# Kernel optimization log

Hardware: AMD Instinct MI355X
Metric: run time of the kernel (lower is better)

Reference implementation:

```python
import jax, jax.numpy as jnp
import numpy as np

NEG_SLOPE = 0.1

def lrelu(x):
    return jnp.where(x >= 0, x, NEG_SLOPE * x)

def conv1d(x, w, b, stride=2):
    # x: [N, C_in, W], w: [C_out, C_in, K], VALID padding, given stride
    y = jax.lax.conv_general_dilated(x, w, (stride,), 'VALID',
                                     dimension_numbers=('NCH', 'OIH', 'NCH'))
    return y + b[None, :, None]

def setup_inputs() -> dict:
    key = jax.random.key(0)
    ks = jax.random.split(key, 16)
    N_NODES = 50000
    N_EDGES = 4950000
    POS_C, CONV_C, CONV_W = 3, 3, 151
    HID, OUT = 256, 1
    W2 = 37  # width after two stride-2 k=3 convs on 151
    IN_G = POS_C + W2  # 40

    def lin_init(k, fan_out, fan_in):
        s = 1.0 / np.sqrt(fan_in)
        k1, k2 = jax.random.split(k)
        return (jax.random.uniform(k1, (fan_out, fan_in), jnp.float32, -s, s),
                jax.random.uniform(k2, (fan_out,), jnp.float32, -s, s))

    pose = jax.random.normal(ks[0], (N_NODES, POS_C), jnp.float32)
    views = jax.random.normal(ks[1], (N_NODES, CONV_C, CONV_W), jnp.float32)
    edge_index = jax.random.randint(ks[2], (2, N_EDGES), 0, N_NODES, jnp.int64)

    # encoder1: Conv1d(3 -> 9, k=3, s=2); encoder2: Conv1d(9 -> 1, k=3, s=2)
    s1 = 1.0 / np.sqrt(CONV_C * 3)
    w_e1 = jax.random.uniform(ks[3], (CONV_C ** 2, CONV_C, 3), jnp.float32, -s1, s1)
    b_e1 = jax.random.uniform(ks[4], (CONV_C ** 2,), jnp.float32, -s1, s1)
    s2 = 1.0 / np.sqrt(CONV_C ** 2 * 3)
    w_e2 = jax.random.uniform(ks[5], (1, CONV_C ** 2, 3), jnp.float32, -s2, s2)
    b_e2 = jax.random.uniform(ks[6], (1,), jnp.float32, -s2, s2)

    # GraphConv: lin_rel (with bias) on aggregated neighbors, lin_root (no bias) on self
    w_rel, b_rel = lin_init(ks[7], HID, IN_G)
    w_root, _ = lin_init(ks[8], HID, IN_G)

    w_l1, b_l1 = lin_init(ks[9], HID, HID)
    w_l2, b_l2 = lin_init(ks[10], HID, HID)
    w_l3, b_l3 = lin_init(ks[11], HID, HID)
    w_pred, b_pred = lin_init(ks[12], OUT, HID)

    return dict(pose=pose, views=views, edge_index=edge_index,
                w_e1=w_e1, b_e1=b_e1, w_e2=w_e2, b_e2=b_e2,
                w_rel=w_rel, b_rel=b_rel, w_root=w_root,
                w_l1=w_l1, b_l1=b_l1, w_l2=w_l2, b_l2=b_l2,
                w_l3=w_l3, b_l3=b_l3, w_pred=w_pred, b_pred=b_pred)

def reference(pose, views, edge_index, w_e1, b_e1, w_e2, b_e2,
              w_rel, b_rel, w_root,
              w_l1, b_l1, w_l2, b_l2, w_l3, b_l3, w_pred, b_pred):
    n_nodes = pose.shape[0]
    # view encoder
    v = lrelu(conv1d(views, w_e1, b_e1))          # [N, 9, 75]
    v = lrelu(conv1d(v, w_e2, b_e2))              # [N, 1, 37]
    x = jnp.concatenate([pose, v[:, 0, :]], axis=1)  # [N, 40]
    # GraphConv (aggr='add'): out = lin_rel(sum_{j->i} x_j) + lin_root(x_i)
    src, dst = edge_index[0], edge_index[1]
    agg = jax.ops.segment_sum(x[src], dst, num_segments=n_nodes)  # [N, 40]
    h = lrelu(agg @ w_rel.T + b_rel + x @ w_root.T)               # [N, 256]
    # MLP stack (dropout is identity in eval mode)
    h = lrelu(h @ w_l1.T + b_l1)
    h = lrelu(h @ w_l2.T + b_l2)
    h = lrelu(h @ w_l3.T + b_l3)
    return h @ w_pred.T + b_pred  # [N, 1]
```

## Files before the change

### kernel.cpp

```cpp
#include <hip/hip_runtime.h>
#include <hip/hip_fp16.h>

#define NEG_SLOPE 0.1f
__device__ __forceinline__ float lrelu(float v) { return fmaxf(v, NEG_SLOPE * v); }

constexpr int CAP = 8704;
constexpr int EPB = 8192;

typedef __attribute__((ext_vector_type(8))) short short8;
typedef __attribute__((ext_vector_type(4))) float f32x4;

__device__ __forceinline__ unsigned short f2bf(float f) {
    union { float f; unsigned u; } v; v.f = f;
    const unsigned r = v.u + 0x7FFF + ((v.u >> 16) & 1);
    return (unsigned short)(r >> 16);
}
__device__ __forceinline__ float bf2f(unsigned short h) {
    union { unsigned u; float f; } v; v.u = ((unsigned)h) << 16;
    return v.f;
}

__global__ __launch_bounds__(256) void encoder_kernel(
        const float* __restrict__ pose,
        const float* __restrict__ views,
        const float* __restrict__ w1, const float* __restrict__ b1,
        const float* __restrict__ w2, const float* __restrict__ b2,
        const float* __restrict__ w_l1, const float* __restrict__ w_l2,
        const float* __restrict__ w_l3, const float* __restrict__ w_rel,
        const float* __restrict__ w_root,
        unsigned short* __restrict__ Wb1, unsigned short* __restrict__ Wb2,
        unsigned short* __restrict__ Wb3, unsigned short* __restrict__ Wg,
        int* __restrict__ gcur,
        unsigned short* __restrict__ xHi, unsigned short* __restrict__ xLo,
        __half* __restrict__ xh, int N)
{
    __shared__ float s_w1[81];
    __shared__ float s_b1[9];
    __shared__ float s_w2[27];
    __shared__ float s_b2[1];
    __shared__ float s_c1[4][9][80];

    const int t = threadIdx.x;

    if (blockIdx.x < 256) {
        const int i = blockIdx.x * 256 + t;
        Wb1[i] = f2bf(w_l1[i]);
        Wb2[i] = f2bf(w_l2[i]);
        Wb3[i] = f2bf(w_l3[i]);
        if (i < 40960) {
            const int m = i / 160, c = i % 160;
            const int k = c % 80;
            const float v = (k < 40) ? w_rel[m * 40 + k] : w_root[m * 40 + (k - 40)];
            Wg[i] = f2bf(v);
        }
        if (i < 1024) gcur[i] = 0;
        if (i < 40) xh[(size_t)N * 40 + i] = __float2half(0.f);
    }

    if (t < 81) s_w1[t] = w1[t];
    if (t >= 96 && t < 105) s_b1[t - 96] = b1[t - 96];
    if (t >= 128 && t < 155) s_w2[t - 128] = w2[t - 128];
    if (t == 240) s_b2[0] = b2[0];
    __syncthreads();

    const int nb = blockIdx.x * 4;

    #pragma unroll
    for (int pass = 0; pass < 2; pass++) {
        const int task = pass * 256 + t;
        if (task < 300) {
            const int ln = task / 75;
            const int p  = task % 75;
            const int n  = min(nb + ln, N - 1);
            const float* __restrict__ vin = views + (size_t)n * 453 + 2 * p;
            float e[3], o[3], e1[3];
            #pragma unroll
            for (int ic = 0; ic < 3; ic++) {
                const float* ci = vin + ic * 151;
                e[ic] = ci[0]; o[ic] = ci[1]; e1[ic] = ci[2];
            }
            const int didx = (p & 1) * 40 + (p >> 1);
            #pragma unroll
            for (int oc = 0; oc < 9; oc++) {
                float v = s_b1[oc];
                #pragma unroll
                for (int ic = 0; ic < 3; ic++)
                    v += s_w1[oc * 9 + ic * 3 + 0] * e[ic]
                       + s_w1[oc * 9 + ic * 3 + 1] * o[ic]
                       + s_w1[oc * 9 + ic * 3 + 2] * e1[ic];
                s_c1[ln][oc][didx] = lrelu(v);
            }
        }
    }
    __syncthreads();

    if (t < 160) {
        const int ln = t / 40, f = t % 40;
        const int n  = min(nb + ln, N - 1);
        float outv;
        if (f < 3) {
            outv = pose[(size_t)n * 3 + f];
        } else {
            const int ow = f - 3;
            float v = s_b2[0];
            #pragma unroll
            for (int ic = 0; ic < 9; ic++)
                v += s_w2[ic * 3 + 0] * s_c1[ln][ic][ow]
                   + s_w2[ic * 3 + 1] * s_c1[ln][ic][40 + ow]
                   + s_w2[ic * 3 + 2] * s_c1[ln][ic][ow + 1];
            outv = lrelu(v);
        }
        const unsigned short hi = f2bf(outv);
        const unsigned short lo = f2bf(outv - bf2f(hi));
        xHi[(size_t)n * 40 + f] = hi;
        xLo[(size_t)n * 40 + f] = lo;
        xh[(size_t)n * 40 + f] = __float2half(outv);
    }
}

__global__ __launch_bounds__(512) void bin_kernel(
        const int* __restrict__ ei, int* __restrict__ gcur,
        int* __restrict__ pairs, int E, int NB)
{
    __shared__ int s_hist[1024];
    __shared__ int s_loff[1024];
    __shared__ int s_base[1024];
    __shared__ int s_wave8[8];
    __shared__ int s_pk[EPB];
    __shared__ unsigned short s_bkt[EPB];
    const int t = threadIdx.x;
    const int lane = t & 63, wid = t >> 6;
    const int e0 = blockIdx.x * EPB + t * 16;
    const int tot = min(E - blockIdx.x * EPB, EPB);

    for (int i = t; i < 1024; i += 512) s_hist[i] = 0;
    __syncthreads();

    int pk[16], mt[16];
    auto proc = [&](int j, int sv, int dv) {
        const int b = dv >> 6;
        const int r = atomicAdd(&s_hist[b], 1);
        pk[j] = sv * 80 | ((dv & 63) << 22);
        mt[j] = b | (r << 10);
    };

    if (e0 + 16 <= E) {
        #pragma unroll
        for (int q = 0; q < 4; q++) {
            const int4 sv = *(const int4*)(ei + e0 + 4 * q);
            const int4 dv = *(const int4*)(ei + E + e0 + 4 * q);
            proc(4 * q + 0, sv.x, dv.x);
            proc(4 * q + 1, sv.y, dv.y);
            proc(4 * q + 2, sv.z, dv.z);
            proc(4 * q + 3, sv.w, dv.w);
        }
    } else {
        #pragma unroll
        for (int j = 0; j < 16; j++) {
            mt[j] = -1;
            const int e = e0 + j;
            if (e < E) proc(j, ei[e], ei[E + e]);
        }
    }
    __syncthreads();

    int carry = 0;
    #pragma unroll
    for (int base = 0; base < 1024; base += 512) {
        const int i = base + t;
        const int v = s_hist[i];
        int sc = v;
        #pragma unroll
        for (int d = 1; d < 64; d <<= 1) {
            const int u = __shfl_up(sc, d);
            if (lane >= d) sc += u;
        }
        if (lane == 63) s_wave8[wid] = sc;
        __syncthreads();
        if (wid == 0) {
            int wv = (lane < 8) ? s_wave8[lane] : 0;
            #pragma unroll
            for (int d = 1; d < 8; d <<= 1) {
                const int u = __shfl_up(wv, d);
                if (lane >= d) wv += u;
            }
            if (lane < 8) s_wave8[lane] = wv;
        }
        __syncthreads();
        const int waveoff = (wid > 0) ? s_wave8[wid - 1] : 0;
        s_loff[i] = carry + waveoff + sc - v;
        const int chunk_tot = s_wave8[7];
        __syncthreads();
        carry += chunk_tot;
    }

    for (int i = t; i < NB; i += 512) {
        const int c = s_hist[i];
        if (c > 0) s_base[i] = atomicAdd(&gcur[i], c);
    }
    __syncthreads();

    #pragma unroll
    for (int j = 0; j < 16; j++) {
        if (mt[j] >= 0) {
            const int b = mt[j] & 1023;
            const int pos = s_loff[b] + (mt[j] >> 10);
            s_pk[pos] = pk[j];
            s_bkt[pos] = (unsigned short)b;
        }
    }
    __syncthreads();

    for (int i = t; i < tot; i += 512) {
        const int b = s_bkt[i];
        const int p = s_base[b] + (i - s_loff[b]);
        if (p < CAP) pairs[b * CAP + p] = s_pk[i];
    }
}

__global__ void bucket_sort_kernel(const int* __restrict__ gcur,
                                   const int* __restrict__ pairs,
                                   int* __restrict__ sorted,
                                   int* __restrict__ node_start,
                                   int* __restrict__ node_cnt, int N)
{
    __shared__ int s_cnt[64], s_off[64], s_cur[64];
    const int b = blockIdx.x;
    const int t = threadIdx.x;
    const int cnt = min(gcur[b], CAP);
    const int* __restrict__ pr = pairs + b * CAP;
    int* __restrict__ so = sorted + (size_t)b * CAP;

    if (t < 64) s_cnt[t] = 0;
    __syncthreads();
    for (int i = t; i < cnt; i += 256)
        atomicAdd(&s_cnt[pr[i] >> 22], 1);
    __syncthreads();

    if (t < 64) {
        const int c = s_cnt[t];
        const int p = ((c + 23) / 24) * 24;
        int sc = p;
        #pragma unroll
        for (int d = 1; d < 64; d <<= 1) {
            const int u = __shfl_up(sc, d);
            if (t >= d) sc += u;
        }
        const int excl = sc - p;
        s_off[t] = excl;
        s_cur[t] = excl;
        node_start[b * 64 + t] = b * CAP + excl;
        node_cnt[b * 64 + t] = c;
    }
    __syncthreads();

    if (t < 64) {
        const int e0 = s_off[t] + s_cnt[t];
        const int e1 = s_off[t] + ((s_cnt[t] + 23) / 24) * 24;
        for (int i = e0; i < e1 && i < CAP; i++) so[i] = N * 80;
    }
    for (int i = t; i < cnt; i += 256) {
        const int p = pr[i];
        const int pos = atomicAdd(&s_cur[p >> 22], 1);
        if (pos < CAP) so[pos] = p & 0x3FFFFF;
    }
}

__global__ void gather_sum_kernel(const int* __restrict__ sorted,
                                  const int* __restrict__ node_start,
                                  const int* __restrict__ node_cnt,
                                  const __half* __restrict__ xh,
                                  unsigned short* __restrict__ aggHi,
                                  unsigned short* __restrict__ aggLo, int N)
{
    const int n = blockIdx.x * 4 + (threadIdx.x >> 6);
    const int lane = threadIdx.x & 63;
    if (n >= N) return;

    const int start = node_start[n];
    const int cntp = ((node_cnt[n] + 23) / 24) * 24;
    const int slot = min(lane / 10, 5);
    const int f4 = lane % 10;
    const int* __restrict__ srt = sorted + start + slot;
    const char* __restrict__ xb = (const char*)xh + f4 * 8;

    float ax = 0.f, ay = 0.f, az = 0.f, aw = 0.f;
    for (int e = 0; e < cntp; e += 24) {
        const int o0 = srt[e];
        const int o1 = srt[e + 6];
        const int o2 = srt[e + 12];
        const int o3 = srt[e + 18];
        const uint2 u0 = *(const uint2*)(xb + o0);
        const uint2 u1 = *(const uint2*)(xb + o1);
        const uint2 u2 = *(const uint2*)(xb + o2);
        const uint2 u3 = *(const uint2*)(xb + o3);
        union { unsigned u; __half2 h; } c;
        float2 f;
        c.u = u0.x; f = __half22float2(c.h); ax += f.x; ay += f.y;
        c.u = u0.y; f = __half22float2(c.h); az += f.x; aw += f.y;
        c.u = u1.x; f = __half22float2(c.h); ax += f.x; ay += f.y;
        c.u = u1.y; f = __half22float2(c.h); az += f.x; aw += f.y;
        c.u = u2.x; f = __half22float2(c.h); ax += f.x; ay += f.y;
        c.u = u2.y; f = __half22float2(c.h); az += f.x; aw += f.y;
        c.u = u3.x; f = __half22float2(c.h); ax += f.x; ay += f.y;
        c.u = u3.y; f = __half22float2(c.h); az += f.x; aw += f.y;
    }

    float rx = ax, ry = ay, rz = az, rw = aw;
    #pragma unroll
    for (int s = 10; s <= 50; s += 10) {
        rx += __shfl(ax, f4 + s);
        ry += __shfl(ay, f4 + s);
        rz += __shfl(az, f4 + s);
        rw += __shfl(aw, f4 + s);
    }
    if (lane < 10) {
        ushort4 hi, lo;
        hi.x = f2bf(rx); lo.x = f2bf(rx - bf2f(hi.x));
        hi.y = f2bf(ry); lo.y = f2bf(ry - bf2f(hi.y));
        hi.z = f2bf(rz); lo.z = f2bf(rz - bf2f(hi.z));
        hi.w = f2bf(rw); lo.w = f2bf(rw - bf2f(hi.w));
        *(ushort4*)(aggHi + (size_t)n * 40 + f4 * 4) = hi;
        *(ushort4*)(aggLo + (size_t)n * 40 + f4 * 4) = lo;
    }
}

__global__ void graphconv_mfma_kernel(const unsigned short* __restrict__ aggHi,
                                      const unsigned short* __restrict__ aggLo,
                                      const unsigned short* __restrict__ xHi,
                                      const unsigned short* __restrict__ xLo,
                                      const unsigned short* __restrict__ Wg,
                                      const float* __restrict__ b,
                                      unsigned short* __restrict__ C, int N)
{
    __shared__ __align__(16) unsigned short aT[64 * 168];
    const int t = threadIdx.x;
    const int n0 = blockIdx.x * 64;
    const int wave = t >> 6, lane = t & 63, q = lane >> 4, l16 = lane & 15;

    for (int u = t; u < 640; u += 256) {
        const int row = u / 10, c = (u % 10) * 4;
        const int srow = min(n0 + row, N - 1);
        const size_t off = (size_t)srow * 40 + c;
        const ushort4 ha = *(const ushort4*)(aggHi + off);
        const ushort4 hx = *(const ushort4*)(xHi + off);
        const ushort4 la = *(const ushort4*)(aggLo + off);
        const ushort4 lx = *(const ushort4*)(xLo + off);
        unsigned short* rp = aT + row * 168;
        *(ushort4*)(rp + c)       = ha;
        *(ushort4*)(rp + 40 + c)  = hx;
        *(ushort4*)(rp + 80 + c)  = la;
        *(ushort4*)(rp + 120 + c) = lx;
    }
    __syncthreads();

    f32x4 acc[4][4] = {};
    for (int k0 = 0; k0 < 160; k0 += 32) {
        short8 af[4], wf[4];
        #pragma unroll
        for (int nt = 0; nt < 4; nt++)
            af[nt] = *(const short8*)(aT + (nt * 16 + l16) * 168 + k0 + q * 8);
        #pragma unroll
        for (int mt = 0; mt < 4; mt++)
            wf[mt] = *(const short8*)(Wg + (wave * 64 + mt * 16 + l16) * 160 + k0 + q * 8);
        #pragma unroll
        for (int nt = 0; nt < 4; nt++)
            #pragma unroll
            for (int mt = 0; mt < 4; mt++)
                acc[nt][mt] = __builtin_amdgcn_mfma_f32_16x16x32_bf16(af[nt], wf[mt], acc[nt][mt], 0, 0, 0);
    }

    float bias[4];
    #pragma unroll
    for (int mt = 0; mt < 4; mt++) bias[mt] = b[wave * 64 + mt * 16 + l16];

    #pragma unroll
    for (int nt = 0; nt < 4; nt++)
        #pragma unroll
        for (int r = 0; r < 4; r++) {
            const int row = n0 + nt * 16 + q * 4 + r;
            if (row >= N) continue;
            #pragma unroll
            for (int mt = 0; mt < 4; mt++) {
                const int col = wave * 64 + mt * 16 + l16;
                C[(size_t)row * 256 + col] = f2bf(lrelu(acc[nt][mt][r] + bias[mt]));
            }
        }
}

__global__ void mlp_mfma_kernel(const unsigned short* __restrict__ A,
                                const unsigned short* __restrict__ W,
                                const float* __restrict__ b,
                                unsigned short* __restrict__ C, int N)
{
    __shared__ __align__(16) unsigned short aT[64 * 264];
    const int t = threadIdx.x;
    const int n0 = blockIdx.x * 64;
    const int wave = t >> 6, lane = t & 63, q = lane >> 4, l16 = lane & 15;

    #pragma unroll
    for (int i = 0; i < 8; i++) {
        const int u = t + 256 * i;
        const int row = u >> 5, c16 = u & 31;
        const int srow = min(n0 + row, N - 1);
        *(uint4*)(aT + row * 264 + c16 * 8) = *(const uint4*)(A + (size_t)srow * 256 + c16 * 8);
    }
    __syncthreads();

    f32x4 acc[4][4] = {};
    const unsigned short* wbase = W + (wave * 64 + l16) * 256 + q * 8;
    for (int k0 = 0; k0 < 256; k0 += 32) {
        short8 af[4], wf[4];
        #pragma unroll
        for (int nt = 0; nt < 4; nt++)
            af[nt] = *(const short8*)(aT + (nt * 16 + l16) * 264 + k0 + q * 8);
        #pragma unroll
        for (int mt = 0; mt < 4; mt++)
            wf[mt] = *(const short8*)(wbase + mt * 16 * 256 + k0);
        #pragma unroll
        for (int nt = 0; nt < 4; nt++)
            #pragma unroll
            for (int mt = 0; mt < 4; mt++)
                acc[nt][mt] = __builtin_amdgcn_mfma_f32_16x16x32_bf16(af[nt], wf[mt], acc[nt][mt], 0, 0, 0);
    }

    float bias[4];
    #pragma unroll
    for (int mt = 0; mt < 4; mt++) bias[mt] = b[wave * 64 + mt * 16 + l16];

    #pragma unroll
    for (int nt = 0; nt < 4; nt++)
        #pragma unroll
        for (int r = 0; r < 4; r++) {
            const int row = n0 + nt * 16 + q * 4 + r;
            if (row >= N) continue;
            #pragma unroll
            for (int mt = 0; mt < 4; mt++) {
                const int col = wave * 64 + mt * 16 + l16;
                C[(size_t)row * 256 + col] = f2bf(lrelu(acc[nt][mt][r] + bias[mt]));
            }
        }
}

__global__ void mlp_pred_kernel(const unsigned short* __restrict__ A,
                                const unsigned short* __restrict__ W,
                                const float* __restrict__ b,
                                const float* __restrict__ w_pred,
                                const float* __restrict__ b_pred,
                                float* __restrict__ out, int N)
{
    __shared__ __align__(16) unsigned short aT[64 * 264];
    __shared__ float s_part[4][64];
    const int t = threadIdx.x;
    const int n0 = blockIdx.x * 64;
    const int wave = t >> 6, lane = t & 63, q = lane >> 4, l16 = lane & 15;

    #pragma unroll
    for (int i = 0; i < 8; i++) {
        const int u = t + 256 * i;
        const int row = u >> 5, c16 = u & 31;
        const int srow = min(n0 + row, N - 1);
        *(uint4*)(aT + row * 264 + c16 * 8) = *(const uint4*)(A + (size_t)srow * 256 + c16 * 8);
    }
    __syncthreads();

    f32x4 acc[4][4] = {};
    const unsigned short* wbase = W + (wave * 64 + l16) * 256 + q * 8;
    for (int k0 = 0; k0 < 256; k0 += 32) {
        short8 af[4], wf[4];
        #pragma unroll
        for (int nt = 0; nt < 4; nt++)
            af[nt] = *(const short8*)(aT + (nt * 16 + l16) * 264 + k0 + q * 8);
        #pragma unroll
        for (int mt = 0; mt < 4; mt++)
            wf[mt] = *(const short8*)(wbase + mt * 16 * 256 + k0);
        #pragma unroll
        for (int nt = 0; nt < 4; nt++)
            #pragma unroll
            for (int mt = 0; mt < 4; mt++)
                acc[nt][mt] = __builtin_amdgcn_mfma_f32_16x16x32_bf16(af[nt], wf[mt], acc[nt][mt], 0, 0, 0);
    }

    float bias[4], wp[4];
    #pragma unroll
    for (int mt = 0; mt < 4; mt++) {
        const int col = wave * 64 + mt * 16 + l16;
        bias[mt] = b[col];
        wp[mt] = w_pred[col];
    }

    #pragma unroll
    for (int nt = 0; nt < 4; nt++)
        #pragma unroll
        for (int r = 0; r < 4; r++) {
            float p = 0.f;
            #pragma unroll
            for (int mt = 0; mt < 4; mt++)
                p += lrelu(acc[nt][mt][r] + bias[mt]) * wp[mt];
            p += __shfl_xor(p, 1);
            p += __shfl_xor(p, 2);
            p += __shfl_xor(p, 4);
            p += __shfl_xor(p, 8);
            if (l16 == 0) s_part[wave][nt * 16 + q * 4 + r] = p;
        }
    __syncthreads();

    if (t < 64) {
        const int row = n0 + t;
        if (row < N)
            out[row] = s_part[0][t] + s_part[1][t] + s_part[2][t] + s_part[3][t] + b_pred[0];
    }
}

extern "C" void kernel_launch(void* const* d_in, const int* in_sizes, int n_in,
                              void* d_out, int out_size, void* d_ws, size_t ws_size,
                              hipStream_t stream)
{
    const float* pose   = (const float*)d_in[0];
    const float* views  = (const float*)d_in[1];
    const int*   ei     = (const int*)d_in[2];
    const float* w_e1   = (const float*)d_in[3];
    const float* b_e1   = (const float*)d_in[4];
    const float* w_e2   = (const float*)d_in[5];
    const float* b_e2   = (const float*)d_in[6];
    const float* w_rel  = (const float*)d_in[7];
    const float* b_rel  = (const float*)d_in[8];
    const float* w_root = (const float*)d_in[9];
    const float* w_l1   = (const float*)d_in[10];
    const float* b_l1   = (const float*)d_in[11];
    const float* w_l2   = (const float*)d_in[12];
    const float* b_l2   = (const float*)d_in[13];
    const float* w_l3   = (const float*)d_in[14];
    const float* b_l3   = (const float*)d_in[15];
    const float* w_pred = (const float*)d_in[16];
    const float* b_pred = (const float*)d_in[17];
    float* out = (float*)d_out;

    const int N = in_sizes[0] / 3;
    const int E = in_sizes[2] / 2;
    const int NB = (N + 63) >> 6;
    const int NBLK = (N + 63) / 64;

    unsigned short* xHi = (unsigned short*)d_ws;
    unsigned short* xLo = xHi + (size_t)N * 40;
    unsigned short* aggHi = xLo + (size_t)N * 40;
    unsigned short* aggLo = aggHi + (size_t)N * 40;
    __half* xh = (__half*)(aggLo + (size_t)N * 40);
    int* pairs  = (int*)(xh + (size_t)(N + 1) * 40 + 24);
    int* sorted = pairs + (size_t)NB * CAP;
    unsigned short* hb0 = (unsigned short*)pairs;
    unsigned short* hb1 = (unsigned short*)sorted;
    int* gcur       = sorted + (size_t)NB * CAP;
    int* node_start = gcur + 1024;
    int* node_cnt   = node_start + NB * 64;
    unsigned short* Wb1 = (unsigned short*)(node_cnt + NB * 64);
    unsigned short* Wb2 = Wb1 + 256 * 256;
    unsigned short* Wb3 = Wb2 + 256 * 256;
    unsigned short* Wg  = Wb3 + 256 * 256;

    encoder_kernel<<<(N + 3) / 4, 256, 0, stream>>>(
        pose, views, w_e1, b_e1, w_e2, b_e2,
        w_l1, w_l2, w_l3, w_rel, w_root,
        Wb1, Wb2, Wb3, Wg, gcur, xHi, xLo, xh, N);

    bin_kernel<<<(E + EPB - 1) / EPB, 512, 0, stream>>>(ei, gcur, pairs, E, NB);
    bucket_sort_kernel<<<NB, 256, 0, stream>>>(gcur, pairs, sorted, node_start, node_cnt, N);
    gather_sum_kernel<<<NB * 16, 256, 0, stream>>>(sorted, node_start, node_cnt, xh, aggHi, aggLo, N);

    graphconv_mfma_kernel<<<NBLK, 256, 0, stream>>>(aggHi, aggLo, xHi, xLo, Wg, b_rel, hb0, N);
    mlp_mfma_kernel<<<NBLK, 256, 0, stream>>>(hb0, Wb1, b_l1, hb1, N);
    mlp_mfma_kernel<<<NBLK, 256, 0, stream>>>(hb1, Wb2, b_l2, hb0, N);
    mlp_pred_kernel<<<NBLK, 256, 0, stream>>>(hb0, Wb3, b_l3, w_pred, b_pred, out, N);
}
```

Before: 391.2 us.

## Fuse graphconv and MLP GEMMs into one kernel, merge encoder with edge binning

Chains the graphconv GEMM and the three MLP layers inside one kernel, keeping each 64-row activation tile in LDS between layers. This removes the global write and read of the 256-wide hidden activations and three kernel launches. It also merges the encoder and edge-binning kernels into one launch using block-index dispatch over a shared LDS union, and zeroes the bucket counters with a memset. The trade-off is that the GEMM chain is serialized per block with extra barriers, and the merged launch uses larger blocks and more LDS for encoder blocks.

```diff
diff --git a/kernel.cpp b/kernel.cpp
--- a/kernel.cpp
+++ b/kernel.cpp
@@ -20,9 +20,21 @@
     return v.f;
 }
 
-__global__ __launch_bounds__(256) void encoder_kernel(
-        const float* __restrict__ pose,
-        const float* __restrict__ views,
+struct BinSmem {
+    int hist[1024], loff[1024], base[1024];
+    int wave8[8];
+    int pk[EPB];
+    unsigned short bkt[EPB];
+};
+struct EncSmem {
+    float w1[81], b1v[9], w2[27], b2v[1];
+    float c1[8][9][80];
+};
+
+__global__ __launch_bounds__(512) void enc_bin_kernel(
+        const int* __restrict__ ei, int* __restrict__ gcur,
+        int* __restrict__ pairs, int E, int NB, int NBIN,
+        const float* __restrict__ pose, const float* __restrict__ views,
         const float* __restrict__ w1, const float* __restrict__ b1,
         const float* __restrict__ w2, const float* __restrict__ b2,
         const float* __restrict__ w_l1, const float* __restrict__ w_l2,
@@ -30,20 +42,109 @@
         const float* __restrict__ w_root,
         unsigned short* __restrict__ Wb1, unsigned short* __restrict__ Wb2,
         unsigned short* __restrict__ Wb3, unsigned short* __restrict__ Wg,
-        int* __restrict__ gcur,
         unsigned short* __restrict__ xHi, unsigned short* __restrict__ xLo,
         __half* __restrict__ xh, int N)
 {
-    __shared__ float s_w1[81];
-    __shared__ float s_b1[9];
-    __shared__ float s_w2[27];
-    __shared__ float s_b2[1];
-    __shared__ float s_c1[4][9][80];
-
+    __shared__ __align__(16) char smem_raw[sizeof(BinSmem)];
     const int t = threadIdx.x;
 
-    if (blockIdx.x < 256) {
-        const int i = blockIdx.x * 256 + t;
+    if (blockIdx.x < (unsigned)NBIN) {
+        BinSmem& sm = *reinterpret_cast<BinSmem*>(smem_raw);
+        const int lane = t & 63, wid = t >> 6;
+        const int e0 = blockIdx.x * EPB + t * 16;
+        const int tot = min(E - (int)blockIdx.x * EPB, EPB);
+
+        for (int i = t; i < 1024; i += 512) sm.hist[i] = 0;
+        __syncthreads();
+
+        int pk[16], mt[16];
+        auto proc = [&](int j, int sv, int dv) {
+            const int b = dv >> 6;
+            const int r = atomicAdd(&sm.hist[b], 1);
+            pk[j] = sv * 80 | ((dv & 63) << 22);
+            mt[j] = b | (r << 10);
+        };
+
+        if (e0 + 16 <= E) {
+            #pragma unroll
+            for (int q = 0; q < 4; q++) {
+                const int4 sv = *(const int4*)(ei + e0 + 4 * q);
+                const int4 dv = *(const int4*)(ei + E + e0 + 4 * q);
+                proc(4 * q + 0, sv.x, dv.x);
+                proc(4 * q + 1, sv.y, dv.y);
+                proc(4 * q + 2, sv.z, dv.z);
+                proc(4 * q + 3, sv.w, dv.w);
+            }
+        } else {
+            #pragma unroll
+            for (int j = 0; j < 16; j++) {
+                mt[j] = -1;
+                const int e = e0 + j;
+                if (e < E) proc(j, ei[e], ei[E + e]);
+            }
+        }
+        __syncthreads();
+
+        int carry = 0;
+        #pragma unroll
+        for (int base = 0; base < 1024; base += 512) {
+            const int i = base + t;
+            const int v = sm.hist[i];
+            int sc = v;
+            #pragma unroll
+            for (int d = 1; d < 64; d <<= 1) {
+                const int u = __shfl_up(sc, d);
+                if (lane >= d) sc += u;
+            }
+            if (lane == 63) sm.wave8[wid] = sc;
+            __syncthreads();
+            if (wid == 0) {
+                int wv = (lane < 8) ? sm.wave8[lane] : 0;
+                #pragma unroll
+                for (int d = 1; d < 8; d <<= 1) {
+                    const int u = __shfl_up(wv, d);
+                    if (lane >= d) wv += u;
+                }
+                if (lane < 8) sm.wave8[lane] = wv;
+            }
+            __syncthreads();
+            const int waveoff = (wid > 0) ? sm.wave8[wid - 1] : 0;
+            sm.loff[i] = carry + waveoff + sc - v;
+            const int chunk_tot = sm.wave8[7];
+            __syncthreads();
+            carry += chunk_tot;
+        }
+
+        for (int i = t; i < NB; i += 512) {
+            const int c = sm.hist[i];
+            if (c > 0) sm.base[i] = atomicAdd(&gcur[i], c);
+        }
+        __syncthreads();
+
+        #pragma unroll
+        for (int j = 0; j < 16; j++) {
+            if (mt[j] >= 0) {
+                const int b = mt[j] & 1023;
+                const int pos = sm.loff[b] + (mt[j] >> 10);
+                sm.pk[pos] = pk[j];
+                sm.bkt[pos] = (unsigned short)b;
+            }
+        }
+        __syncthreads();
+
+        for (int i = t; i < tot; i += 512) {
+            const int b = sm.bkt[i];
+            const int p = sm.base[b] + (i - sm.loff[b]);
+            if (p < CAP) pairs[b * CAP + p] = sm.pk[i];
+        }
+        return;
+    }
+
+    EncSmem& sm = *reinterpret_cast<EncSmem*>(smem_raw);
+    const int eb = blockIdx.x - NBIN;
+
+    if (eb < 128) {
+        const int i = eb * 512 + t;
         Wb1[i] = f2bf(w_l1[i]);
         Wb2[i] = f2bf(w_l2[i]);
         Wb3[i] = f2bf(w_l3[i]);
@@ -53,22 +154,21 @@
             const float v = (k < 40) ? w_rel[m * 40 + k] : w_root[m * 40 + (k - 40)];
             Wg[i] = f2bf(v);
         }
-        if (i < 1024) gcur[i] = 0;
-        if (i < 40) xh[(size_t)N * 40 + i] = __float2half(0.f);
-    }
-
-    if (t < 81) s_w1[t] = w1[t];
-    if (t >= 96 && t < 105) s_b1[t - 96] = b1[t - 96];
-    if (t >= 128 && t < 155) s_w2[t - 128] = w2[t - 128];
-    if (t == 240) s_b2[0] = b2[0];
+        if (eb == 0 && t < 40) xh[(size_t)N * 40 + t] = __float2half(0.f);
+    }
+
+    if (t < 81) sm.w1[t] = w1[t];
+    if (t >= 96 && t < 105) sm.b1v[t - 96] = b1[t - 96];
+    if (t >= 128 && t < 155) sm.w2[t - 128] = w2[t - 128];
+    if (t == 240) sm.b2v[0] = b2[0];
     __syncthreads();
 
-    const int nb = blockIdx.x * 4;
+    const int nb = eb * 8;
 
     #pragma unroll
     for (int pass = 0; pass < 2; pass++) {
-        const int task = pass * 256 + t;
-        if (task < 300) {
+        const int task = pass * 512 + t;
+        if (task < 600) {
             const int ln = task / 75;
             const int p  = task % 75;
             const int n  = min(nb + ln, N - 1);
@@ -82,19 +182,19 @@
             const int didx = (p & 1) * 40 + (p >> 1);
             #pragma unroll
             for (int oc = 0; oc < 9; oc++) {
-                float v = s_b1[oc];
+                float v = sm.b1v[oc];
                 #pragma unroll
                 for (int ic = 0; ic < 3; ic++)
-                    v += s_w1[oc * 9 + ic * 3 + 0] * e[ic]
-                       + s_w1[oc * 9 + ic * 3 + 1] * o[ic]
-                       + s_w1[oc * 9 + ic * 3 + 2] * e1[ic];
-                s_c1[ln][oc][didx] = lrelu(v);
+                    v += sm.w1[oc * 9 + ic * 3 + 0] * e[ic]
+                       + sm.w1[oc * 9 + ic * 3 + 1] * o[ic]
+                       + sm.w1[oc * 9 + ic * 3 + 2] * e1[ic];
+                sm.c1[ln][oc][didx] = lrelu(v);
             }
         }
     }
     __syncthreads();
 
-    if (t < 160) {
+    if (t < 320) {
         const int ln = t / 40, f = t % 40;
         const int n  = min(nb + ln, N - 1);
         float outv;
@@ -102,12 +202,12 @@
             outv = pose[(size_t)n * 3 + f];
         } else {
             const int ow = f - 3;
-            float v = s_b2[0];
+            float v = sm.b2v[0];
             #pragma unroll
             for (int ic = 0; ic < 9; ic++)
-                v += s_w2[ic * 3 + 0] * s_c1[ln][ic][ow]
-                   + s_w2[ic * 3 + 1] * s_c1[ln][ic][40 + ow]
-                   + s_w2[ic * 3 + 2] * s_c1[ln][ic][ow + 1];
+                v += sm.w2[ic * 3 + 0] * sm.c1[ln][ic][ow]
+                   + sm.w2[ic * 3 + 1] * sm.c1[ln][ic][40 + ow]
+                   + sm.w2[ic * 3 + 2] * sm.c1[ln][ic][ow + 1];
             outv = lrelu(v);
         }
         const unsigned short hi = f2bf(outv);
@@ -115,106 +215,6 @@
         xHi[(size_t)n * 40 + f] = hi;
         xLo[(size_t)n * 40 + f] = lo;
         xh[(size_t)n * 40 + f] = __float2half(outv);
-    }
-}
-
-__global__ __launch_bounds__(512) void bin_kernel(
-        const int* __restrict__ ei, int* __restrict__ gcur,
-        int* __restrict__ pairs, int E, int NB)
-{
-    __shared__ int s_hist[1024];
-    __shared__ int s_loff[1024];
-    __shared__ int s_base[1024];
-    __shared__ int s_wave8[8];
-    __shared__ int s_pk[EPB];
-    __shared__ unsigned short s_bkt[EPB];
-    const int t = threadIdx.x;
-    const int lane = t & 63, wid = t >> 6;
-    const int e0 = blockIdx.x * EPB + t * 16;
-    const int tot = min(E - blockIdx.x * EPB, EPB);
-
-    for (int i = t; i < 1024; i += 512) s_hist[i] = 0;
-    __syncthreads();
-
-    int pk[16], mt[16];
-    auto proc = [&](int j, int sv, int dv) {
-        const int b = dv >> 6;
-        const int r = atomicAdd(&s_hist[b], 1);
-        pk[j] = sv * 80 | ((dv & 63) << 22);
-        mt[j] = b | (r << 10);
-    };
-
-    if (e0 + 16 <= E) {
-        #pragma unroll
-        for (int q = 0; q < 4; q++) {
-            const int4 sv = *(const int4*)(ei + e0 + 4 * q);
-            const int4 dv = *(const int4*)(ei + E + e0 + 4 * q);
-            proc(4 * q + 0, sv.x, dv.x);
-            proc(4 * q + 1, sv.y, dv.y);
-            proc(4 * q + 2, sv.z, dv.z);
-            proc(4 * q + 3, sv.w, dv.w);
-        }
-    } else {
-        #pragma unroll
-        for (int j = 0; j < 16; j++) {
-            mt[j] = -1;
-            const int e = e0 + j;
-            if (e < E) proc(j, ei[e], ei[E + e]);
-        }
-    }
-    __syncthreads();
-
-    int carry = 0;
-    #pragma unroll
-    for (int base = 0; base < 1024; base += 512) {
-        const int i = base + t;
-        const int v = s_hist[i];
-        int sc = v;
-        #pragma unroll
-        for (int d = 1; d < 64; d <<= 1) {
-            const int u = __shfl_up(sc, d);
-            if (lane >= d) sc += u;
-        }
-        if (lane == 63) s_wave8[wid] = sc;
-        __syncthreads();
-        if (wid == 0) {
-            int wv = (lane < 8) ? s_wave8[lane] : 0;
-            #pragma unroll
-            for (int d = 1; d < 8; d <<= 1) {
-                const int u = __shfl_up(wv, d);
-                if (lane >= d) wv += u;
-            }
-            if (lane < 8) s_wave8[lane] = wv;
-        }
-        __syncthreads();
-        const int waveoff = (wid > 0) ? s_wave8[wid - 1] : 0;
-        s_loff[i] = carry + waveoff + sc - v;
-        const int chunk_tot = s_wave8[7];
-        __syncthreads();
-        carry += chunk_tot;
-    }
-
-    for (int i = t; i < NB; i += 512) {
-        const int c = s_hist[i];
-        if (c > 0) s_base[i] = atomicAdd(&gcur[i], c);
-    }
-    __syncthreads();
-
-    #pragma unroll
-    for (int j = 0; j < 16; j++) {
-        if (mt[j] >= 0) {
-            const int b = mt[j] & 1023;
-            const int pos = s_loff[b] + (mt[j] >> 10);
-            s_pk[pos] = pk[j];
-            s_bkt[pos] = (unsigned short)b;
-        }
-    }
-    __syncthreads();
-
-    for (int i = t; i < tot; i += 512) {
-        const int b = s_bkt[i];
-        const int p = s_base[b] + (i - s_loff[b]);
-        if (p < CAP) pairs[b * CAP + p] = s_pk[i];
     }
 }
 
@@ -325,129 +325,62 @@
     }
 }
 
-__global__ void graphconv_mfma_kernel(const unsigned short* __restrict__ aggHi,
-                                      const unsigned short* __restrict__ aggLo,
-                                      const unsigned short* __restrict__ xHi,
-                                      const unsigned short* __restrict__ xLo,
-                                      const unsigned short* __restrict__ Wg,
-                                      const float* __restrict__ b,
-                                      unsigned short* __restrict__ C, int N)
-{
-    __shared__ __align__(16) unsigned short aT[64 * 168];
-    const int t = threadIdx.x;
-    const int n0 = blockIdx.x * 64;
-    const int wave = t >> 6, lane = t & 63, q = lane >> 4, l16 = lane & 15;
-
-    for (int u = t; u < 640; u += 256) {
-        const int row = u / 10, c = (u % 10) * 4;
-        const int srow = min(n0 + row, N - 1);
-        const size_t off = (size_t)srow * 40 + c;
-        const ushort4 ha = *(const ushort4*)(aggHi + off);
-        const ushort4 hx = *(const ushort4*)(xHi + off);
-        const ushort4 la = *(const ushort4*)(aggLo + off);
-        const ushort4 lx = *(const ushort4*)(xLo + off);
-        unsigned short* rp = aT + row * 168;
-        *(ushort4*)(rp + c)       = ha;
-        *(ushort4*)(rp + 40 + c)  = hx;
-        *(ushort4*)(rp + 80 + c)  = la;
-        *(ushort4*)(rp + 120 + c) = lx;
-    }
-    __syncthreads();
-
-    f32x4 acc[4][4] = {};
-    for (int k0 = 0; k0 < 160; k0 += 32) {
+__device__ __forceinline__ void gemm_tile(const unsigned short* __restrict__ aT,
+                                          const unsigned short* __restrict__ W,
+                                          int wstride, int K,
+                                          int wave, int l16, int q,
+                                          f32x4 acc[4][4])
+{
+    for (int k0 = 0; k0 < K; k0 += 32) {
         short8 af[4], wf[4];
         #pragma unroll
         for (int nt = 0; nt < 4; nt++)
-            af[nt] = *(const short8*)(aT + (nt * 16 + l16) * 168 + k0 + q * 8);
+            af[nt] = *(const short8*)(aT + (nt * 16 + l16) * 264 + k0 + q * 8);
         #pragma unroll
         for (int mt = 0; mt < 4; mt++)
-            wf[mt] = *(const short8*)(Wg + (wave * 64 + mt * 16 + l16) * 160 + k0 + q * 8);
+            wf[mt] = *(const short8*)(W + (wave * 64 + mt * 16 + l16) * wstride + k0 + q * 8);
         #pragma unroll
         for (int nt = 0; nt < 4; nt++)
             #pragma unroll
             for (int mt = 0; mt < 4; mt++)
                 acc[nt][mt] = __builtin_amdgcn_mfma_f32_16x16x32_bf16(af[nt], wf[mt], acc[nt][mt], 0, 0, 0);
     }
-
+}
+
+__device__ __forceinline__ void epi_to_lds(f32x4 acc[4][4], const float* __restrict__ b,
+                                           unsigned short* __restrict__ aT,
+                                           int wave, int l16, int q)
+{
     float bias[4];
     #pragma unroll
     for (int mt = 0; mt < 4; mt++) bias[mt] = b[wave * 64 + mt * 16 + l16];
-
     #pragma unroll
     for (int nt = 0; nt < 4; nt++)
         #pragma unroll
-        for (int r = 0; r < 4; r++) {
-            const int row = n0 + nt * 16 + q * 4 + r;
-            if (row >= N) continue;
+        for (int r = 0; r < 4; r++)
             #pragma unroll
             for (int mt = 0; mt < 4; mt++) {
+                const int row = nt * 16 + q * 4 + r;
                 const int col = wave * 64 + mt * 16 + l16;
-                C[(size_t)row * 256 + col] = f2bf(lrelu(acc[nt][mt][r] + bias[mt]));
-            }
-        }
-}
-
-__global__ void mlp_mfma_kernel(const unsigned short* __restrict__ A,
-                                const unsigned short* __restrict__ W,
-                                const float* __restrict__ b,
-                                unsigned short* __restrict__ C, int N)
-{
-    __shared__ __align__(16) unsigned short aT[64 * 264];
-    const int t = threadIdx.x;
-    const int n0 = blockIdx.x * 64;
-    const int wave = t >> 6, lane = t & 63, q = lane >> 4, l16 = lane & 15;
-
-    #pragma unroll
-    for (int i = 0; i < 8; i++) {
-        const int u = t + 256 * i;
-        const int row = u >> 5, c16 = u & 31;
-        const int srow = min(n0 + row, N - 1);
-        *(uint4*)(aT + row * 264 + c16 * 8) = *(const uint4*)(A + (size_t)srow * 256 + c16 * 8);
-    }
-    __syncthreads();
-
-    f32x4 acc[4][4] = {};
-    const unsigned short* wbase = W + (wave * 64 + l16) * 256 + q * 8;
-    for (int k0 = 0; k0 < 256; k0 += 32) {
-        short8 af[4], wf[4];
-        #pragma unroll
-        for (int nt = 0; nt < 4; nt++)
-            af[nt] = *(const short8*)(aT + (nt * 16 + l16) * 264 + k0 + q * 8);
-        #pragma unroll
-        for (int mt = 0; mt < 4; mt++)
-            wf[mt] = *(const short8*)(wbase + mt * 16 * 256 + k0);
-        #pragma unroll
-        for (int nt = 0; nt < 4; nt++)
-            #pragma unroll
-            for (int mt = 0; mt < 4; mt++)
-                acc[nt][mt] = __builtin_amdgcn_mfma_f32_16x16x32_bf16(af[nt], wf[mt], acc[nt][mt], 0, 0, 0);
-    }
-
-    float bias[4];
-    #pragma unroll
-    for (int mt = 0; mt < 4; mt++) bias[mt] = b[wave * 64 + mt * 16 + l16];
-
-    #pragma unroll
-    for (int nt = 0; nt < 4; nt++)
-        #pragma unroll
-        for (int r = 0; r < 4; r++) {
-            const int row = n0 + nt * 16 + q * 4 + r;
-            if (row >= N) continue;
-            #pragma unroll
-            for (int mt = 0; mt < 4; mt++) {
-                const int col = wave * 64 + mt * 16 + l16;
-                C[(size_t)row * 256 + col] = f2bf(lrelu(acc[nt][mt][r] + bias[mt]));
-            }
-        }
-}
-
-__global__ void mlp_pred_kernel(const unsigned short* __restrict__ A,
-                                const unsigned short* __restrict__ W,
-                                const float* __restrict__ b,
-                                const float* __restrict__ w_pred,
-                                const float* __restrict__ b_pred,
-                                float* __restrict__ out, int N)
+                aT[row * 264 + col] = f2bf(lrelu(acc[nt][mt][r] + bias[mt]));
+            }
+}
+
+__global__ void fused_gemm_kernel(const unsigned short* __restrict__ aggHi,
+                                  const unsigned short* __restrict__ aggLo,
+                                  const unsigned short* __restrict__ xHi,
+                                  const unsigned short* __restrict__ xLo,
+                                  const unsigned short* __restrict__ Wg,
+                                  const float* __restrict__ b_rel,
+                                  const unsigned short* __restrict__ Wb1,
+                                  const float* __restrict__ b_l1,
+                                  const unsigned short* __restrict__ Wb2,
+                                  const float* __restrict__ b_l2,
+                                  const unsigned short* __restrict__ Wb3,
+                                  const float* __restrict__ b_l3,
+                                  const float* __restrict__ w_pred,
+                                  const float* __restrict__ b_pred,
+                                  float* __restrict__ out, int N)
 {
     __shared__ __align__(16) unsigned short aT[64 * 264];
     __shared__ float s_part[4][64];
@@ -455,60 +388,71 @@
     const int n0 = blockIdx.x * 64;
     const int wave = t >> 6, lane = t & 63, q = lane >> 4, l16 = lane & 15;
 
-    #pragma unroll
-    for (int i = 0; i < 8; i++) {
-        const int u = t + 256 * i;
-        const int row = u >> 5, c16 = u & 31;
+    for (int u = t; u < 640; u += 256) {
+        const int row = u / 10, c = (u % 10) * 4;
         const int srow = min(n0 + row, N - 1);
-        *(uint4*)(aT + row * 264 + c16 * 8) = *(const uint4*)(A + (size_t)srow * 256 + c16 * 8);
+        const size_t off = (size_t)srow * 40 + c;
+        unsigned short* rp = aT + row * 264;
+        *(ushort4*)(rp + c)       = *(const ushort4*)(aggHi + off);
+        *(ushort4*)(rp + 40 + c)  = *(const ushort4*)(xHi + off);
+        *(ushort4*)(rp + 80 + c)  = *(const ushort4*)(aggLo + off);
+        *(ushort4*)(rp + 120 + c) = *(const ushort4*)(xLo + off);
     }
     __syncthreads();
 
-    f32x4 acc[4][4] = {};
-    const unsigned short* wbase = W + (wave * 64 + l16) * 256 + q * 8;
-    for (int k0 = 0; k0 < 256; k0 += 32) {
-        short8 af[4], wf[4];
+    {
+        f32x4 acc[4][4] = {};
+        gemm_tile(aT, Wg, 160, 160, wave, l16, q, acc);
+        __syncthreads();
+        epi_to_lds(acc, b_rel, aT, wave, l16, q);
+        __syncthreads();
+    }
+    {
+        f32x4 acc[4][4] = {};
+        gemm_tile(aT, Wb1, 256, 256, wave, l16, q, acc);
+        __syncthreads();
+        epi_to_lds(acc, b_l1, aT, wave, l16, q);
+        __syncthreads();
+    }
+    {
+        f32x4 acc[4][4] = {};
+        gemm_tile(aT, Wb2, 256, 256, wave, l16, q, acc);
+        __syncthreads();
+        epi_to_lds(acc, b_l2, aT, wave, l16, q);
+        __syncthreads();
+    }
+    {
+        f32x4 acc[4][4] = {};
+        gemm_tile(aT, Wb3, 256, 256, wave, l16, q, acc);
+
+        float bias[4], wp[4];
+        #pragma unroll
+        for (int mt = 0; mt < 4; mt++) {
+            const int col = wave * 64 + mt * 16 + l16;
+            bias[mt] = b_l3[col];
+            wp[mt] = w_pred[col];
+        }
         #pragma unroll
         for (int nt = 0; nt < 4; nt++)
-            af[nt] = *(const short8*)(aT + (nt * 16 + l16) * 264 + k0 + q * 8);
-        #pragma unroll
-        for (int mt = 0; mt < 4; mt++)
-            wf[mt] = *(const short8*)(wbase + mt * 16 * 256 + k0);
-        #pragma unroll
-        for (int nt = 0; nt < 4; nt++)
-            #pragma unroll
-            for (int mt = 0; mt < 4; mt++)
-                acc[nt][mt] = __builtin_amdgcn_mfma_f32_16x16x32_bf16(af[nt], wf[mt], acc[nt][mt], 0, 0, 0);
-    }
-
-    float bias[4], wp[4];
-    #pragma unroll
-    for (int mt = 0; mt < 4; mt++) {
-        const int col = wave * 64 + mt * 16 + l16;
-        bias[mt] = b[col];
-        wp[mt] = w_pred[col];
-    }
-
-    #pragma unroll
-    for (int nt = 0; nt < 4; nt++)
-        #pragma unroll
-        for (int r = 0; r < 4; r++) {
-            float p = 0.f;
-            #pragma unroll
-            for (int mt = 0; mt < 4; mt++)
-                p += lrelu(acc[nt][mt][r] + bias[mt]) * wp[mt];
-            p += __shfl_xor(p, 1);
-            p += __shfl_xor(p, 2);
-            p += __shfl_xor(p, 4);
-            p += __shfl_xor(p, 8);
-            if (l16 == 0) s_part[wave][nt * 16 + q * 4 + r] = p;
-        }
-    __syncthreads();
-
-    if (t < 64) {
-        const int row = n0 + t;
-        if (row < N)
-            out[row] = s_part[0][t] + s_part[1][t] + s_part[2][t] + s_part[3][t] + b_pred[0];
+            #pragma unroll
+            for (int r = 0; r < 4; r++) {
+                float p = 0.f;
+                #pragma unroll
+                for (int mt = 0; mt < 4; mt++)
+                    p += lrelu(acc[nt][mt][r] + bias[mt]) * wp[mt];
+                p += __shfl_xor(p, 1);
+                p += __shfl_xor(p, 2);
+                p += __shfl_xor(p, 4);
+                p += __shfl_xor(p, 8);
+                if (l16 == 0) s_part[wave][nt * 16 + q * 4 + r] = p;
+            }
+        __syncthreads();
+
+        if (t < 64) {
+            const int row = n0 + t;
+            if (row < N)
+                out[row] = s_part[0][t] + s_part[1][t] + s_part[2][t] + s_part[3][t] + b_pred[0];
+        }
     }
 }
 
@@ -539,6 +483,8 @@
     const int N = in_sizes[0] / 3;
     const int E = in_sizes[2] / 2;
     const int NB = (N + 63) >> 6;
+    const int NBIN = (E + EPB - 1) / EPB;
+    const int ENCB = (N + 7) / 8;
     const int NBLK = (N + 63) / 64;
 
     unsigned short* xHi = (unsigned short*)d_ws;
@@ -548,8 +494,6 @@
     __half* xh = (__half*)(aggLo + (size_t)N * 40);
     int* pairs  = (int*)(xh + (size_t)(N + 1) * 40 + 24);
     int* sorted = pairs + (size_t)NB * CAP;
-    unsigned short* hb0 = (unsigned short*)pairs;
-    unsigned short* hb1 = (unsigned short*)sorted;
     int* gcur       = sorted + (size_t)NB * CAP;
     int* node_start = gcur + 1024;
     int* node_cnt   = node_start + NB * 64;
@@ -558,17 +502,20 @@
     unsigned short* Wb3 = Wb2 + 256 * 256;
     unsigned short* Wg  = Wb3 + 256 * 256;
 
-    encoder_kernel<<<(N + 3) / 4, 256, 0, stream>>>(
+    hipMemsetAsync(gcur, 0, 1024 * sizeof(int), stream);
+
+    enc_bin_kernel<<<NBIN + ENCB, 512, 0, stream>>>(
+        ei, gcur, pairs, E, NB, NBIN,
         pose, views, w_e1, b_e1, w_e2, b_e2,
         w_l1, w_l2, w_l3, w_rel, w_root,
-        Wb1, Wb2, Wb3, Wg, gcur, xHi, xLo, xh, N);
-
-    bin_kernel<<<(E + EPB - 1) / EPB, 512, 0, stream>>>(ei, gcur, pairs, E, NB);
+        Wb1, Wb2, Wb3, Wg,
+        xHi, xLo, xh, N);
+
     bucket_sort_kernel<<<NB, 256, 0, stream>>>(gcur, pairs, sorted, node_start, node_cnt, N);
     gather_sum_kernel<<<NB * 16, 256, 0, stream>>>(sorted, node_start, node_cnt, xh, aggHi, aggLo, N);
 
-    graphconv_mfma_kernel<<<NBLK, 256, 0, stream>>>(aggHi, aggLo, xHi, xLo, Wg, b_rel, hb0, N);
-    mlp_mfma_kernel<<<NBLK, 256, 0, stream>>>(hb0, Wb1, b_l1, hb1, N);
-    mlp_mfma_kernel<<<NBLK, 256, 0, stream>>>(hb1, Wb2, b_l2, hb0, N);
-    mlp_pred_kernel<<<NBLK, 256, 0, stream>>>(hb0, Wb3, b_l3, w_pred, b_pred, out, N);
-}
+    fused_gemm_kernel<<<NBLK, 256, 0, stream>>>(
+        aggHi, aggLo, xHi, xLo, Wg, b_rel,
+        Wb1, b_l1, Wb2, b_l2, Wb3, b_l3,
+        w_pred, b_pred, out, N);
+}
```

Result: faster. 370.4 us (-5.3%).
